# Kernel optimization log

Hardware: AMD Instinct MI355X
Metric: run time of the kernel (lower is better)

## Reference

```python
import jax, jax.numpy as jnp
import numpy as np
import math

BATCH, CLS, ATT_DIM, IMG_DIM = 256, 500, 1024, 1024
ATT_HC, HIDDEN_C = 256, 1024
T_TEMP = 10.0
DEGREE = 30
THRESH = math.cos(math.pi * DEGREE / 180.0)
NEG = -9.0e15


def setup_inputs() -> dict:
    key = jax.random.key(0)
    ks = jax.random.split(key, 9)
    inp = {
        "image_feats": jax.random.normal(ks[0], (BATCH, IMG_DIM), dtype=jnp.float32),
        "attributes": jax.random.normal(ks[1], (CLS, ATT_DIM), dtype=jnp.float32),
        "unused": 0,
        # learned parameters (kaiming-like scaling)
        "att_g": jax.random.normal(ks[2], (ATT_DIM, ATT_HC), dtype=jnp.float32) / math.sqrt(ATT_DIM),
        "img_w": jax.random.normal(ks[3], (IMG_DIM, HIDDEN_C), dtype=jnp.float32) / math.sqrt(IMG_DIM),
        "sem_w": jax.random.normal(ks[4], (ATT_DIM, HIDDEN_C), dtype=jnp.float32) / math.sqrt(ATT_DIM),
        "sem_b": jax.random.normal(ks[5], (1, HIDDEN_C), dtype=jnp.float32) / math.sqrt(IMG_DIM),
        "fc_w": jax.random.normal(ks[6], (1, HIDDEN_C), dtype=jnp.float32) / math.sqrt(HIDDEN_C),
        "fc_b": jax.random.normal(ks[7], (1,), dtype=jnp.float32) / math.sqrt(HIDDEN_C),
    }
    return inp


def _get_new_attribute(attributes, att_g):
    # project attributes, cosine similarity between all class pairs
    g = attributes @ att_g                                    # [cls, att_hC]
    gn = g / jnp.linalg.norm(g, axis=1, keepdims=True)        # row-normalize
    sim = gn @ gn.T                                           # [cls, cls] cosine sims
    raw = jnp.where(sim > THRESH, sim, NEG)                   # angular-threshold mask
    attention = jax.nn.softmax(raw * T_TEMP, axis=1)          # [cls, cls]
    return attention @ attributes                             # [cls, att_dim]


def reference(image_feats, attributes, unused, att_g, img_w, sem_w, sem_b, fc_w, fc_b):
    att_outs = _get_new_attribute(attributes, att_g)          # [cls, att_dim]
    # factor the broadcast: identical math to matmul on expanded tensors
    img_h = image_feats @ img_w                               # [batch, hidden]
    sem_h = att_outs @ sem_w                                  # [cls, hidden]
    hidden = jax.nn.relu(img_h[:, None, :] + sem_h[None, :, :] + sem_b[None, :, :])  # [batch, cls, hidden]
    out = jnp.einsum('bch,h->bc', hidden, fc_w[0]) + fc_b[0]  # [batch, cls]
    return out
```

## Files before the change

### kernel.cpp

```cpp
#include <hip/hip_runtime.h>
#include <math.h>

#define BATCH 256
#define CLS 500
#define T_TEMP_ 10.0f
#define THRESH_ 0.86602540378443864676f
#define NEGV -9.0e15f

typedef __attribute__((ext_vector_type(8))) short short8;
typedef __attribute__((ext_vector_type(8))) unsigned short u16x8;
typedef __attribute__((ext_vector_type(4))) unsigned short u16x4;
typedef __attribute__((ext_vector_type(4))) float f32x4;
typedef __attribute__((ext_vector_type(2))) float f32x2;

static __device__ __forceinline__ unsigned short f2bf(float x) {
    unsigned int u = __builtin_bit_cast(unsigned int, x);
    u += 0x7fff + ((u >> 16) & 1);
    return (unsigned short)(u >> 16);
}
static __device__ __forceinline__ float bf2f(unsigned short v) {
    return __builtin_bit_cast(float, (unsigned int)v << 16);
}
static __device__ __forceinline__ float fel(const float4& v, int j) { return (&v.x)[j]; }
static __device__ __forceinline__ u16x8 pack8(const float4& a, const float4& b) {
    u16x8 o;
    o[0] = f2bf(a.x); o[1] = f2bf(a.y); o[2] = f2bf(a.z); o[3] = f2bf(a.w);
    o[4] = f2bf(b.x); o[5] = f2bf(b.y); o[6] = f2bf(b.z); o[7] = f2bf(b.w);
    return o;
}

__global__ __launch_bounds__(256) void g_norm_kernel(
    const float* __restrict__ attrs, const float* __restrict__ attg,
    float* __restrict__ gpart, unsigned short* __restrict__ gn_bf,
    unsigned int* __restrict__ cnt)
{
    __shared__ unsigned short As[64][40];
    __shared__ unsigned short Bs[128][40];
    __shared__ float red[4];
    __shared__ unsigned int rank_s;
    const int t = threadIdx.x;
    const int bid = blockIdx.x;
    const int mt = bid >> 4, nt = (bid >> 3) & 1, split = bid & 7;
    const int n0 = nt * 128, ar0 = mt * 64, k0 = split * 128;

    const int w = t >> 6, lane = t & 63;
    const int wr = w >> 1, wc = w & 1;
    const int fr = lane & 15, kg = lane >> 4;
    const int as_row = t >> 2, as_kq = t & 3;
    const int bs_nc = (t & 31) * 4, bs_kr = t >> 5;

    f32x4 acc[2][4];
    #pragma unroll
    for (int i = 0; i < 2; ++i)
        #pragma unroll
        for (int j = 0; j < 4; ++j) acc[i][j] = (f32x4){0.f, 0.f, 0.f, 0.f};

    for (int kb = k0; kb < k0 + 128; kb += 32) {
        {
            const int gr = ar0 + as_row;
            float4 v0 = make_float4(0.f,0.f,0.f,0.f), v1 = v0;
            if (gr < CLS) {
                const float* ap = &attrs[(size_t)gr * 1024 + kb + as_kq * 8];
                v0 = *(const float4*)ap; v1 = *(const float4*)(ap + 4);
            }
            *(u16x8*)&As[as_row][as_kq * 8] = pack8(v0, v1);
        }
        {
            const float* bp = &attg[(size_t)(kb + bs_kr * 4) * 256 + n0 + bs_nc];
            float4 r0 = *(const float4*)(bp);
            float4 r1 = *(const float4*)(bp + 256);
            float4 r2 = *(const float4*)(bp + 512);
            float4 r3 = *(const float4*)(bp + 768);
            #pragma unroll
            for (int j = 0; j < 4; ++j) {
                unsigned int lo = (unsigned int)f2bf(fel(r0, j)) | ((unsigned int)f2bf(fel(r1, j)) << 16);
                unsigned int hi = (unsigned int)f2bf(fel(r2, j)) | ((unsigned int)f2bf(fel(r3, j)) << 16);
                uint2 u2; u2.x = lo; u2.y = hi;
                *(uint2*)&Bs[bs_nc + j][bs_kr * 4] = u2;
            }
        }
        __syncthreads();
        short8 af[2], bfr[4];
        #pragma unroll
        for (int i = 0; i < 2; ++i) af[i] = *(short8*)&As[wr * 32 + i * 16 + fr][kg * 8];
        #pragma unroll
        for (int j = 0; j < 4; ++j) bfr[j] = *(short8*)&Bs[wc * 64 + j * 16 + fr][kg * 8];
        #pragma unroll
        for (int i = 0; i < 2; ++i)
            #pragma unroll
            for (int j = 0; j < 4; ++j)
                acc[i][j] = __builtin_amdgcn_mfma_f32_16x16x32_bf16(af[i], bfr[j], acc[i][j], 0, 0, 0);
        __syncthreads();
    }

    float* Gp = gpart + (size_t)split * (512 * 256);
    const int orow0 = ar0 + wr * 32, ocol0 = n0 + wc * 64;
    #pragma unroll
    for (int i = 0; i < 2; ++i) {
        const int r0 = orow0 + i * 16 + kg * 4;
        #pragma unroll
        for (int j = 0; j < 4; ++j) {
            const int cc = ocol0 + j * 16 + fr;
            #pragma unroll
            for (int r = 0; r < 4; ++r)
                __hip_atomic_store(&Gp[(size_t)(r0 + r) * 256 + cc], acc[i][j][r],
                                   __ATOMIC_RELAXED, __HIP_MEMORY_SCOPE_AGENT);
        }
    }
    asm volatile("s_waitcnt vmcnt(0)" ::: "memory");
    __syncthreads();
    if (t == 0) {
        rank_s = __hip_atomic_fetch_add(&cnt[mt * 32], 1u, __ATOMIC_RELAXED,
                                        __HIP_MEMORY_SCOPE_AGENT);
        while (__hip_atomic_load(&cnt[mt * 32], __ATOMIC_RELAXED,
                                 __HIP_MEMORY_SCOPE_AGENT) < 16u)
            __builtin_amdgcn_s_sleep(1);
    }
    __syncthreads();
    const int rank = (int)rank_s;

    #pragma unroll
    for (int rr4 = 0; rr4 < 4; ++rr4) {
        const int r = mt * 64 + rank * 4 + rr4;
        if (r < CLS) {
            float v = 0.f;
            #pragma unroll
            for (int z = 0; z < 8; ++z)
                v += gpart[(size_t)z * (512 * 256) + (size_t)r * 256 + t];
            float ss = v * v;
            #pragma unroll
            for (int off = 32; off >= 1; off >>= 1) ss += __shfl_down(ss, off);
            if (lane == 0) red[w] = ss;
            __syncthreads();
            const float tot = red[0] + red[1] + red[2] + red[3];
            gn_bf[r * 256 + t] = f2bf(v * (1.f / sqrtf(tot)));
            __syncthreads();
        }
    }
}

__global__ __launch_bounds__(256) void mfma_gemm_bf(
    const unsigned short* __restrict__ A1, int alim1,
    const unsigned short* __restrict__ A2, int a2t0, int alim2,
    const unsigned short* __restrict__ B1, const unsigned short* __restrict__ B2,
    float* __restrict__ C, unsigned short* __restrict__ Cbf,
    int M, int N, int K, int klen)
{
    __shared__ unsigned short As[64][40];
    __shared__ unsigned short Bs[128][40];

    const int t  = threadIdx.x;
    const int bx = blockIdx.x;
    const int n0 = blockIdx.y * 128;
    const int k0 = blockIdx.z * klen;

    const unsigned short* A; const unsigned short* B; int ar0, alim;
    if (bx < a2t0) { A = A1; B = B1; ar0 = bx * 64;          alim = alim1; }
    else           { A = A2; B = B2; ar0 = (bx - a2t0) * 64; alim = alim2; }

    const int w = t >> 6, lane = t & 63;
    const int wr = w >> 1, wc = w & 1;
    const int fr = lane & 15, kg = lane >> 4;

    const int a_row = t >> 2, a_k = (t & 3) * 8;
    const int b_row = t >> 1, b_k = (t & 1) * 16;
    const int gra = ar0 + a_row;
    const int grb = n0 + b_row;
    const bool va = gra < alim;
    const bool vb = grb < N;
    const size_t abase = (size_t)gra * K + a_k;
    const size_t bbase = (size_t)grb * K + b_k;

    u16x8 zz = {0,0,0,0,0,0,0,0};
    u16x8 pa = zz, pb0 = zz, pb1 = zz;
    if (va) pa = *(const u16x8*)&A1[abase + k0];
    if (vb) { pb0 = *(const u16x8*)&B1[bbase + k0]; pb1 = *(const u16x8*)&B1[bbase + k0 + 8]; }

    f32x4 acc[2][4];
    #pragma unroll
    for (int i = 0; i < 2; ++i)
        #pragma unroll
        for (int j = 0; j < 4; ++j) acc[i][j] = (f32x4){0.f, 0.f, 0.f, 0.f};

    for (int kb = k0; kb < k0 + klen; kb += 32) {
        *(u16x8*)&As[a_row][a_k] = pa;
        *(u16x8*)&Bs[b_row][b_k] = pb0;
        *(u16x8*)&Bs[b_row][b_k + 8] = pb1;
        __syncthreads();

        const int kn = kb + 32;
        if (kn < k0 + klen) {
            if (va) pa = *(const u16x8*)&A[abase + kn];
            if (vb) { pb0 = *(const u16x8*)&B[bbase + kn]; pb1 = *(const u16x8*)&B[bbase + kn + 8]; }
        }

        short8 af[2], bfr[4];
        #pragma unroll
        for (int i = 0; i < 2; ++i) af[i] = *(short8*)&As[wr * 32 + i * 16 + fr][kg * 8];
        #pragma unroll
        for (int j = 0; j < 4; ++j) bfr[j] = *(short8*)&Bs[wc * 64 + j * 16 + fr][kg * 8];
        #pragma unroll
        for (int i = 0; i < 2; ++i)
            #pragma unroll
            for (int j = 0; j < 4; ++j)
                acc[i][j] = __builtin_amdgcn_mfma_f32_16x16x32_bf16(af[i], bfr[j], acc[i][j], 0, 0, 0);
        __syncthreads();
    }

    const int orow0 = bx * 64 + wr * 32, ocol0 = n0 + wc * 64;
    if (Cbf) {
        unsigned short* Cw = Cbf + (size_t)blockIdx.z * M * N;
        #pragma unroll
        for (int i = 0; i < 2; ++i) {
            const int r0 = orow0 + i * 16 + kg * 4;
            #pragma unroll
            for (int j = 0; j < 4; ++j) {
                const int cc = ocol0 + j * 16 + fr;
                if (cc >= N) continue;
                #pragma unroll
                for (int r = 0; r < 4; ++r) {
                    const int rr = r0 + r;
                    if (rr < M) Cw[(size_t)rr * N + cc] = f2bf(acc[i][j][r]);
                }
            }
        }
    } else {
        float* Cw = C + (gridDim.z > 1 ? (size_t)blockIdx.z * M * N : 0);
        #pragma unroll
        for (int i = 0; i < 2; ++i) {
            const int r0 = orow0 + i * 16 + kg * 4;
            #pragma unroll
            for (int j = 0; j < 4; ++j) {
                const int cc = ocol0 + j * 16 + fr;
                if (cc >= N) continue;
                #pragma unroll
                for (int r = 0; r < 4; ++r) {
                    const int rr = r0 + r;
                    if (rr < M) Cw[(size_t)rr * N + cc] = acc[i][j][r];
                }
            }
        }
    }
}

__global__ __launch_bounds__(256) void softmax_att_kernel(
    const float* __restrict__ sim, const float* __restrict__ attrs,
    unsigned short* __restrict__ att_outs)
{
    const int c = blockIdx.x, t = threadIdx.x;
    __shared__ float p_s[512];
    __shared__ float redm[4];
    __shared__ float reds[4];

    const float d0 = sim[(size_t)c * CLS + t];
    const float d1 = (t + 256 < CLS) ? sim[(size_t)c * CLS + t + 256] : NEGV;

    float vmax = fmaxf((d0 > THRESH_) ? d0 : NEGV, (d1 > THRESH_) ? d1 : NEGV);
    #pragma unroll
    for (int off = 32; off >= 1; off >>= 1) vmax = fmaxf(vmax, __shfl_down(vmax, off));
    const int wave = t >> 6, lane = t & 63;
    if (lane == 0) redm[wave] = vmax;
    __syncthreads();
    const float m = fmaxf(fmaxf(redm[0], redm[1]), fmaxf(redm[2], redm[3]));

    const float p0 = (d0 > THRESH_) ? expf(T_TEMP_ * (d0 - m)) : 0.f;
    const float p1 = (d1 > THRESH_) ? expf(T_TEMP_ * (d1 - m)) : 0.f;
    p_s[t] = p0;
    p_s[t + 256] = p1;
    float vsum = p0 + p1;
    #pragma unroll
    for (int off = 32; off >= 1; off >>= 1) vsum += __shfl_down(vsum, off);
    if (lane == 0) reds[wave] = vsum;
    __syncthreads();
    const float inv = 1.f / (reds[0] + reds[1] + reds[2] + reds[3]);

    float acc[4] = {0.f, 0.f, 0.f, 0.f};
    for (int base = 0; base < 512; base += 64) {
        const float pv_l = p_s[base + lane];
        unsigned long long mask = __ballot(pv_l > 0.f);
        while (mask) {
            const int l = __ffsll((long long)mask) - 1;
            mask &= mask - 1;
            const int c2 = base + l;
            const float pv = p_s[c2];
            const float* ar = &attrs[(size_t)c2 * 1024 + t];
            #pragma unroll
            for (int j = 0; j < 4; ++j) acc[j] += pv * ar[256 * j];
        }
    }
    #pragma unroll
    for (int j = 0; j < 4; ++j)
        att_outs[(size_t)c * 1024 + t + 256 * j] = f2bf(acc[j] * inv);
}

__global__ __launch_bounds__(256) void hid_kernel(
    const float* __restrict__ imgf, const unsigned short* __restrict__ atto_bf,
    const float* __restrict__ imgw, const float* __restrict__ semw,
    unsigned short* __restrict__ hidP)
{
    __shared__ unsigned short As[64][40];
    __shared__ unsigned short Bs[128][40];
    const int t = threadIdx.x;
    const int mt = blockIdx.x, nt = blockIdx.y, split = blockIdx.z;
    const int n0 = nt * 128, k0 = split * 512;
    const bool img_side = (mt < 4);
    const int ar0 = img_side ? mt * 64 : (mt - 4) * 64;
    const int alim = img_side ? 256 : 500;
    const float* Bf = img_side ? imgw : semw;

    const int w = t >> 6, lane = t & 63;
    const int wr = w >> 1, wc = w & 1;
    const int fr = lane & 15, kg = lane >> 4;
    const int as_row = t >> 2, as_kq = t & 3;
    const int bs_nc = (t & 31) * 4, bs_kr = t >> 5;

    f32x4 acc[2][4];
    #pragma unroll
    for (int i = 0; i < 2; ++i)
        #pragma unroll
        for (int j = 0; j < 4; ++j) acc[i][j] = (f32x4){0.f, 0.f, 0.f, 0.f};

    for (int kb = k0; kb < k0 + 512; kb += 32) {
        {
            const int gr = ar0 + as_row;
            if (img_side) {
                float4 v0 = make_float4(0.f,0.f,0.f,0.f), v1 = v0;
                if (gr < alim) {
                    const float* ap = &imgf[(size_t)gr * 1024 + kb + as_kq * 8];
                    v0 = *(const float4*)ap; v1 = *(const float4*)(ap + 4);
                }
                *(u16x8*)&As[as_row][as_kq * 8] = pack8(v0, v1);
            } else {
                u16x8 pa = {0,0,0,0,0,0,0,0};
                if (gr < alim) pa = *(const u16x8*)&atto_bf[(size_t)gr * 1024 + kb + as_kq * 8];
                *(u16x8*)&As[as_row][as_kq * 8] = pa;
            }
        }
        {
            const float* bp = &Bf[(size_t)(kb + bs_kr * 4) * 1024 + n0 + bs_nc];
            float4 r0 = *(const float4*)(bp);
            float4 r1 = *(const float4*)(bp + 1024);
            float4 r2 = *(const float4*)(bp + 2048);
            float4 r3 = *(const float4*)(bp + 3072);
            #pragma unroll
            for (int j = 0; j < 4; ++j) {
                unsigned int lo = (unsigned int)f2bf(fel(r0, j)) | ((unsigned int)f2bf(fel(r1, j)) << 16);
                unsigned int hi = (unsigned int)f2bf(fel(r2, j)) | ((unsigned int)f2bf(fel(r3, j)) << 16);
                uint2 u2; u2.x = lo; u2.y = hi;
                *(uint2*)&Bs[bs_nc + j][bs_kr * 4] = u2;
            }
        }
        __syncthreads();
        short8 af[2], bfr[4];
        #pragma unroll
        for (int i = 0; i < 2; ++i) af[i] = *(short8*)&As[wr * 32 + i * 16 + fr][kg * 8];
        #pragma unroll
        for (int j = 0; j < 4; ++j) bfr[j] = *(short8*)&Bs[wc * 64 + j * 16 + fr][kg * 8];
        #pragma unroll
        for (int i = 0; i < 2; ++i)
            #pragma unroll
            for (int j = 0; j < 4; ++j)
                acc[i][j] = __builtin_amdgcn_mfma_f32_16x16x32_bf16(af[i], bfr[j], acc[i][j], 0, 0, 0);
        __syncthreads();
    }

    unsigned short* Cw = hidP + (size_t)split * (756 * 1024);
    const int orow0 = mt * 64 + wr * 32, ocol0 = n0 + wc * 64;
    #pragma unroll
    for (int i = 0; i < 2; ++i) {
        const int r0 = orow0 + i * 16 + kg * 4;
        #pragma unroll
        for (int j = 0; j < 4; ++j) {
            const int cc = ocol0 + j * 16 + fr;
            #pragma unroll
            for (int r = 0; r < 4; ++r) {
                const int rr = r0 + r;
                if (rr < 756) Cw[(size_t)rr * 1024 + cc] = f2bf(acc[i][j][r]);
            }
        }
    }
}

__global__ __launch_bounds__(256) void fused_kernel(
    const unsigned short* __restrict__ part, const float* __restrict__ sem_b,
    const float* __restrict__ fc_w, const float* __restrict__ fc_b,
    float* __restrict__ outP, float* __restrict__ out,
    unsigned int* __restrict__ cnt)
{
    __shared__ float imgs[64][68];
    __shared__ float sems[64][68];
    __shared__ float fcs[128];
    __shared__ unsigned int rank_s;
    const size_t pstride = (size_t)756 * 1024;
    const int t = threadIdx.x;
    const int bid = blockIdx.x;
    const int bx = bid & 3, by = (bid >> 2) & 7, bz = bid >> 5;
    const int b0 = bx * 64, c0 = by * 64, h0 = bz * 128;
    const int tb = t >> 4, tc = t & 15;

    if (t < 32) *(float4*)&fcs[t * 4] = *(const float4*)&fc_w[h0 + t * 4];

    f32x2 acc2[4][4];
    #pragma unroll
    for (int i = 0; i < 4; ++i)
        #pragma unroll
        for (int j = 0; j < 4; ++j) acc2[i][j] = (f32x2){0.f, 0.f};

    for (int hs = 0; hs < 2; ++hs) {
        const int hb = h0 + hs * 64;
        #pragma unroll
        for (int i = 0; i < 4; ++i) {
            const int row = (t >> 4) + 16 * i;
            const int col = (t & 15) * 4;
            f32x4 iv = {0.f, 0.f, 0.f, 0.f};
            const unsigned short* pi = &part[(size_t)(b0 + row) * 1024 + hb + col];
            #pragma unroll
            for (int z = 0; z < 2; ++z) {
                u16x4 vz = *(const u16x4*)(pi + (size_t)z * pstride);
                iv[0] += bf2f(vz[0]); iv[1] += bf2f(vz[1]);
                iv[2] += bf2f(vz[2]); iv[3] += bf2f(vz[3]);
            }
            *(f32x4*)&imgs[row][col] = iv;

            f32x4 sv = {0.f, 0.f, 0.f, 0.f};
            if (c0 + row < CLS) {
                const unsigned short* ps2 = &part[(size_t)(256 + c0 + row) * 1024 + hb + col];
                #pragma unroll
                for (int z = 0; z < 2; ++z) {
                    u16x4 vz = *(const u16x4*)(ps2 + (size_t)z * pstride);
                    sv[0] += bf2f(vz[0]); sv[1] += bf2f(vz[1]);
                    sv[2] += bf2f(vz[2]); sv[3] += bf2f(vz[3]);
                }
                const f32x4 bb = *(const f32x4*)&sem_b[hb + col];
                sv += bb;
            }
            *(f32x4*)&sems[row][col] = sv;
        }
        __syncthreads();

        #pragma unroll
        for (int h4 = 0; h4 < 16; ++h4) {
            f32x4 ia[4], sa[4];
            #pragma unroll
            for (int i = 0; i < 4; ++i) ia[i] = *(f32x4*)&imgs[tb + 16 * i][h4 * 4];
            #pragma unroll
            for (int j = 0; j < 4; ++j) sa[j] = *(f32x4*)&sems[tc + 16 * j][h4 * 4];
            const f32x4 wv = *(const f32x4*)&fcs[hs * 64 + h4 * 4];
            #pragma unroll
            for (int e2 = 0; e2 < 2; ++e2) {
                const f32x2 w2 = {wv[2 * e2], wv[2 * e2 + 1]};
                f32x2 ia2[4], sa2[4];
                #pragma unroll
                for (int i = 0; i < 4; ++i) ia2[i] = (f32x2){ia[i][2 * e2], ia[i][2 * e2 + 1]};
                #pragma unroll
                for (int j = 0; j < 4; ++j) sa2[j] = (f32x2){sa[j][2 * e2], sa[j][2 * e2 + 1]};
                #pragma unroll
                for (int i = 0; i < 4; ++i)
                    #pragma unroll
                    for (int j = 0; j < 4; ++j) {
                        f32x2 s = ia2[i] + sa2[j];
                        s = __builtin_elementwise_max(s, (f32x2){0.f, 0.f});
                        acc2[i][j] += s * w2;
                    }
            }
        }
        __syncthreads();
    }

    #pragma unroll
    for (int i = 0; i < 4; ++i) {
        const int b = b0 + tb + 16 * i;
        #pragma unroll
        for (int j = 0; j < 4; ++j) {
            const int cc = c0 + tc + 16 * j;
            if (cc < CLS)
                __hip_atomic_store(&outP[((size_t)bz * BATCH + b) * CLS + cc],
                                   acc2[i][j][0] + acc2[i][j][1],
                                   __ATOMIC_RELAXED, __HIP_MEMORY_SCOPE_AGENT);
        }
    }
    asm volatile("s_waitcnt vmcnt(0)" ::: "memory");
    __syncthreads();
    const int g = bid & 31;
    if (t == 0) {
        rank_s = __hip_atomic_fetch_add(&cnt[g * 32], 1u, __ATOMIC_RELAXED,
                                        __HIP_MEMORY_SCOPE_AGENT);
        while (__hip_atomic_load(&cnt[g * 32], __ATOMIC_RELAXED,
                                 __HIP_MEMORY_SCOPE_AGENT) < 8u)
            __builtin_amdgcn_s_sleep(1);
    }
    __syncthreads();
    const int rank = (int)rank_s;
    const float bias = fc_b[0];
    #pragma unroll
    for (int pass = 0; pass < 2; ++pass) {
        const int row = b0 + rank * 8 + pass * 4 + (t >> 6);
        const int col = c0 + (t & 63);
        if (col < CLS) {
            float s = bias;
            #pragma unroll
            for (int z = 0; z < 8; ++z)
                s += outP[((size_t)z * BATCH + row) * CLS + col];
            out[(size_t)row * CLS + col] = s;
        }
    }
}

extern "C" void kernel_launch(void* const* d_in, const int* in_sizes, int n_in,
                              void* d_out, int out_size, void* d_ws, size_t ws_size,
                              hipStream_t stream)
{
    const float* imgf  = (const float*)d_in[0];
    const float* attrs = (const float*)d_in[1];
    const float* attg  = (const float*)d_in[3];
    const float* imgw  = (const float*)d_in[4];
    const float* semw  = (const float*)d_in[5];
    const float* semb  = (const float*)d_in[6];
    const float* fcw   = (const float*)d_in[7];
    const float* fcb   = (const float*)d_in[8];
    float* out = (float*)d_out;

    char* ws = (char*)d_ws;
    size_t off = 8192;
    auto alloc = [&](size_t b) { size_t o = off; off = (off + b + 255) & ~(size_t)255; return o; };
    unsigned int* cnt1 = (unsigned int*)ws;
    unsigned int* cnt2 = (unsigned int*)(ws + 4096);
    float* gpart          = (float*)(ws + alloc((size_t)8 * 512 * 256 * 4));
    unsigned short* gn_bf = (unsigned short*)(ws + alloc((size_t)500 * 256 * 2));
    float* sim            = (float*)(ws + alloc((size_t)CLS * CLS * 4));
    unsigned short* atto  = (unsigned short*)(ws + alloc((size_t)500 * 1024 * 2));
    unsigned short* hidP  = (unsigned short*)(ws + alloc((size_t)2 * 756 * 1024 * 2));
    float* outP           = (float*)(ws + alloc((size_t)8 * BATCH * CLS * 4));

    hipMemsetAsync(d_ws, 0, 8192, stream);

    g_norm_kernel<<<128, 256, 0, stream>>>(attrs, attg, gpart, gn_bf, cnt1);

    mfma_gemm_bf<<<dim3(8, 4, 1), 256, 0, stream>>>(
        gn_bf, 500, gn_bf, 1000, 500, gn_bf, gn_bf,
        sim, nullptr, 500, 500, 256, 256);

    softmax_att_kernel<<<CLS, 256, 0, stream>>>(sim, attrs, atto);

    hid_kernel<<<dim3(12, 8, 2), 256, 0, stream>>>(imgf, atto, imgw, semw, hidP);

    fused_kernel<<<256, 256, 0, stream>>>(hidP, semb, fcw, fcb, outP, out, cnt2);
}
```

Measured before the change: 74.80 us.

## Replace in-kernel atomic grid barriers with separate reduction kernels

Removes the spin-wait counter barriers from the g-norm and final output kernels. Each is split into a partial-compute kernel plus a separate reduce/finalize kernel, and the workspace memset for the counters is dropped. This gets rid of atomic polling and the dependence on co-residency of blocks. In exchange it adds two extra kernel launches, and the partial buffers make an extra round trip through global memory. It also makes the GEMM prologue load from the selected A/B pointers instead of always A1/B1.

```diff
diff --git a/kernel.cpp b/kernel.cpp
--- a/kernel.cpp
+++ b/kernel.cpp
@@ -29,15 +29,12 @@
     return o;
 }
 
-__global__ __launch_bounds__(256) void g_norm_kernel(
+__global__ __launch_bounds__(256) void gpart_kernel(
     const float* __restrict__ attrs, const float* __restrict__ attg,
-    float* __restrict__ gpart, unsigned short* __restrict__ gn_bf,
-    unsigned int* __restrict__ cnt)
+    float* __restrict__ gpart)
 {
     __shared__ unsigned short As[64][40];
     __shared__ unsigned short Bs[128][40];
-    __shared__ float red[4];
-    __shared__ unsigned int rank_s;
     const int t = threadIdx.x;
     const int bid = blockIdx.x;
     const int mt = bid >> 4, nt = (bid >> 3) & 1, split = bid & 7;
@@ -103,40 +100,28 @@
             const int cc = ocol0 + j * 16 + fr;
             #pragma unroll
             for (int r = 0; r < 4; ++r)
-                __hip_atomic_store(&Gp[(size_t)(r0 + r) * 256 + cc], acc[i][j][r],
-                                   __ATOMIC_RELAXED, __HIP_MEMORY_SCOPE_AGENT);
-        }
-    }
-    asm volatile("s_waitcnt vmcnt(0)" ::: "memory");
+                Gp[(size_t)(r0 + r) * 256 + cc] = acc[i][j][r];
+        }
+    }
+}
+
+__global__ __launch_bounds__(256) void reduce_norm_kernel(
+    const float* __restrict__ part, unsigned short* __restrict__ gn_bf)
+{
+    const int c = blockIdx.x, t = threadIdx.x;
+    float v = 0.f;
+    #pragma unroll
+    for (int z = 0; z < 8; ++z) v += part[(size_t)z * (512 * 256) + c * 256 + t];
+    float ss = v * v;
+    #pragma unroll
+    for (int off = 32; off >= 1; off >>= 1) ss += __shfl_down(ss, off);
+    __shared__ float red[4];
+    const int wave = t >> 6, lane = t & 63;
+    if (lane == 0) red[wave] = ss;
     __syncthreads();
-    if (t == 0) {
-        rank_s = __hip_atomic_fetch_add(&cnt[mt * 32], 1u, __ATOMIC_RELAXED,
-                                        __HIP_MEMORY_SCOPE_AGENT);
-        while (__hip_atomic_load(&cnt[mt * 32], __ATOMIC_RELAXED,
-                                 __HIP_MEMORY_SCOPE_AGENT) < 16u)
-            __builtin_amdgcn_s_sleep(1);
-    }
-    __syncthreads();
-    const int rank = (int)rank_s;
-
-    #pragma unroll
-    for (int rr4 = 0; rr4 < 4; ++rr4) {
-        const int r = mt * 64 + rank * 4 + rr4;
-        if (r < CLS) {
-            float v = 0.f;
-            #pragma unroll
-            for (int z = 0; z < 8; ++z)
-                v += gpart[(size_t)z * (512 * 256) + (size_t)r * 256 + t];
-            float ss = v * v;
-            #pragma unroll
-            for (int off = 32; off >= 1; off >>= 1) ss += __shfl_down(ss, off);
-            if (lane == 0) red[w] = ss;
-            __syncthreads();
-            const float tot = red[0] + red[1] + red[2] + red[3];
-            gn_bf[r * 256 + t] = f2bf(v * (1.f / sqrtf(tot)));
-            __syncthreads();
-        }
-    }
+    const float tot = red[0] + red[1] + red[2] + red[3];
+    const float rn  = 1.f / sqrtf(tot);
+    gn_bf[c * 256 + t] = f2bf(v * rn);
 }
 
 __global__ __launch_bounds__(256) void mfma_gemm_bf(
@@ -173,8 +158,8 @@
 
     u16x8 zz = {0,0,0,0,0,0,0,0};
     u16x8 pa = zz, pb0 = zz, pb1 = zz;
-    if (va) pa = *(const u16x8*)&A1[abase + k0];
-    if (vb) { pb0 = *(const u16x8*)&B1[bbase + k0]; pb1 = *(const u16x8*)&B1[bbase + k0 + 8]; }
+    if (va) pa = *(const u16x8*)&A[abase + k0];
+    if (vb) { pb0 = *(const u16x8*)&B[bbase + k0]; pb1 = *(const u16x8*)&B[bbase + k0 + 8]; }
 
     f32x4 acc[2][4];
     #pragma unroll
@@ -381,22 +366,19 @@
     }
 }
 
-__global__ __launch_bounds__(256) void fused_kernel(
+__global__ __launch_bounds__(256) void fused_out_partial(
     const unsigned short* __restrict__ part, const float* __restrict__ sem_b,
-    const float* __restrict__ fc_w, const float* __restrict__ fc_b,
-    float* __restrict__ outP, float* __restrict__ out,
-    unsigned int* __restrict__ cnt)
+    const float* __restrict__ fc_w, float* __restrict__ outpart)
 {
     __shared__ float imgs[64][68];
     __shared__ float sems[64][68];
     __shared__ float fcs[128];
-    __shared__ unsigned int rank_s;
+
     const size_t pstride = (size_t)756 * 1024;
-    const int t = threadIdx.x;
-    const int bid = blockIdx.x;
-    const int bx = bid & 3, by = (bid >> 2) & 7, bz = bid >> 5;
-    const int b0 = bx * 64, c0 = by * 64, h0 = bz * 128;
+    const int t  = threadIdx.x;
     const int tb = t >> 4, tc = t & 15;
+    const int b0 = blockIdx.x * 64, c0 = blockIdx.y * 64;
+    const int h0 = blockIdx.z * 128;
 
     if (t < 32) *(float4*)&fcs[t * 4] = *(const float4*)&fc_w[h0 + t * 4];
 
@@ -467,6 +449,7 @@
         __syncthreads();
     }
 
+    const int nh = blockIdx.z;
     #pragma unroll
     for (int i = 0; i < 4; ++i) {
         const int b = b0 + tb + 16 * i;
@@ -474,36 +457,22 @@
         for (int j = 0; j < 4; ++j) {
             const int cc = c0 + tc + 16 * j;
             if (cc < CLS)
-                __hip_atomic_store(&outP[((size_t)bz * BATCH + b) * CLS + cc],
-                                   acc2[i][j][0] + acc2[i][j][1],
-                                   __ATOMIC_RELAXED, __HIP_MEMORY_SCOPE_AGENT);
-        }
-    }
-    asm volatile("s_waitcnt vmcnt(0)" ::: "memory");
-    __syncthreads();
-    const int g = bid & 31;
-    if (t == 0) {
-        rank_s = __hip_atomic_fetch_add(&cnt[g * 32], 1u, __ATOMIC_RELAXED,
-                                        __HIP_MEMORY_SCOPE_AGENT);
-        while (__hip_atomic_load(&cnt[g * 32], __ATOMIC_RELAXED,
-                                 __HIP_MEMORY_SCOPE_AGENT) < 8u)
-            __builtin_amdgcn_s_sleep(1);
-    }
-    __syncthreads();
-    const int rank = (int)rank_s;
-    const float bias = fc_b[0];
-    #pragma unroll
-    for (int pass = 0; pass < 2; ++pass) {
-        const int row = b0 + rank * 8 + pass * 4 + (t >> 6);
-        const int col = c0 + (t & 63);
-        if (col < CLS) {
-            float s = bias;
-            #pragma unroll
-            for (int z = 0; z < 8; ++z)
-                s += outP[((size_t)z * BATCH + row) * CLS + col];
-            out[(size_t)row * CLS + col] = s;
-        }
-    }
+                outpart[((size_t)nh * BATCH + b) * CLS + cc] = acc2[i][j][0] + acc2[i][j][1];
+        }
+    }
+}
+
+__global__ __launch_bounds__(256) void finalize_kernel(
+    const float* __restrict__ partial, const float* __restrict__ fc_b,
+    float* __restrict__ out)
+{
+    const int idx = blockIdx.x * 256 + threadIdx.x;
+    if (idx >= BATCH * CLS) return;
+    float s = fc_b[0];
+    #pragma unroll
+    for (int nh = 0; nh < 8; ++nh)
+        s += partial[(size_t)nh * (BATCH * CLS) + idx];
+    out[idx] = s;
 }
 
 extern "C" void kernel_launch(void* const* d_in, const int* in_sizes, int n_in,
@@ -521,10 +490,8 @@
     float* out = (float*)d_out;
 
     char* ws = (char*)d_ws;
-    size_t off = 8192;
+    size_t off = 0;
     auto alloc = [&](size_t b) { size_t o = off; off = (off + b + 255) & ~(size_t)255; return o; };
-    unsigned int* cnt1 = (unsigned int*)ws;
-    unsigned int* cnt2 = (unsigned int*)(ws + 4096);
     float* gpart          = (float*)(ws + alloc((size_t)8 * 512 * 256 * 4));
     unsigned short* gn_bf = (unsigned short*)(ws + alloc((size_t)500 * 256 * 2));
     float* sim            = (float*)(ws + alloc((size_t)CLS * CLS * 4));
@@ -532,17 +499,13 @@
     unsigned short* hidP  = (unsigned short*)(ws + alloc((size_t)2 * 756 * 1024 * 2));
     float* outP           = (float*)(ws + alloc((size_t)8 * BATCH * CLS * 4));
 
-    hipMemsetAsync(d_ws, 0, 8192, stream);
-
-    g_norm_kernel<<<128, 256, 0, stream>>>(attrs, attg, gpart, gn_bf, cnt1);
-
+    gpart_kernel<<<128, 256, 0, stream>>>(attrs, attg, gpart);
+    reduce_norm_kernel<<<CLS, 256, 0, stream>>>(gpart, gn_bf);
     mfma_gemm_bf<<<dim3(8, 4, 1), 256, 0, stream>>>(
         gn_bf, 500, gn_bf, 1000, 500, gn_bf, gn_bf,
         sim, nullptr, 500, 500, 256, 256);
-
     softmax_att_kernel<<<CLS, 256, 0, stream>>>(sim, attrs, atto);
-
     hid_kernel<<<dim3(12, 8, 2), 256, 0, stream>>>(imgf, atto, imgw, semw, hidP);
-
-    fused_kernel<<<256, 256, 0, stream>>>(hidP, semb, fcw, fcb, outP, out, cnt2);
-}
+    fused_out_partial<<<dim3(4, 8, 8), 256, 0, stream>>>(hidP, semb, fcw, outP);
+    finalize_kernel<<<(BATCH * CLS + 255) / 256, 256, 0, stream>>>(outP, fcb, out);
+}
```

Measured after the change: 68.54 us. -8.4%, faster.
